# Kernel tuning notes

Hardware: AMD Instinct MI355X
Metric: run time of the kernel (lower is better)

The kernel has to match this reference:

```python
import jax, jax.numpy as jnp
import numpy as np

V, LAG, H, M, O, B = 32, 1024, 512, 1024, 1, 256


def setup_inputs() -> dict:
    key = jax.random.key(0)
    ks = jax.random.split(key, 10)
    s_ih = 1.0 / np.sqrt(H)
    inputs = jax.random.normal(ks[0], (B, V, LAG, 1), dtype=jnp.float32)
    # per-variable LSTMCell params, stacked over vars; gate order i,f,g,o (torch)
    W_ih = jax.random.uniform(ks[1], (V, 4 * H, LAG), minval=-s_ih, maxval=s_ih, dtype=jnp.float32)
    W_hh = jax.random.uniform(ks[2], (V, 4 * H, H), minval=-s_ih, maxval=s_ih, dtype=jnp.float32)
    b_ih = jax.random.uniform(ks[3], (V, 4 * H), minval=-s_ih, maxval=s_ih, dtype=jnp.float32)
    b_hh = jax.random.uniform(ks[4], (V, 4 * H), minval=-s_ih, maxval=s_ih, dtype=jnp.float32)
    imp_weights = jnp.asarray(np.ones((V,), np.float32) / V + np.random.RandomState(0).normal(0, 1e-5, (V,)).astype(np.float32))
    # xavier-normal linears, bias 0.1 (init_weights)
    mlp1_w = jax.random.normal(ks[5], (M, V * H), dtype=jnp.float32) * np.sqrt(2.0 / (V * H + M))
    mlp1_b = jnp.full((M,), 0.1, dtype=jnp.float32)
    mlp2_w = jax.random.normal(ks[6], (O, M), dtype=jnp.float32) * np.sqrt(2.0 / (M + O))
    mlp2_b = jnp.full((O,), 0.1, dtype=jnp.float32)
    return dict(inputs=inputs, W_ih=W_ih, W_hh=W_hh, b_ih=b_ih, b_hh=b_hh,
                imp_weights=imp_weights, mlp1_w=mlp1_w, mlp1_b=mlp1_b,
                mlp2_w=mlp2_w, mlp2_b=mlp2_b)


def reference(inputs, W_ih, W_hh, b_ih, b_hh, imp_weights, mlp1_w, mlp1_b, mlp2_w, mlp2_b):
    b = inputs.shape[0]
    x = inputs.reshape(b, V, LAG)                      # [B,V,LAG] (view in torch)
    h0 = jnp.zeros((b, V, H), inputs.dtype)           # initial states are zeros
    # single LSTMCell step for all vars at once; gate order i,f,g,o
    gates = (jnp.einsum('bvl,vgl->bvg', x, W_ih)
             + jnp.einsum('bvh,vgh->bvg', h0, W_hh)
             + b_ih[None] + b_hh[None])                # [B,V,4H]
    i, f, g, o = jnp.split(gates, 4, axis=-1)
    c = jax.nn.sigmoid(f) * 0.0 + jax.nn.sigmoid(i) * jnp.tanh(g)  # c0 = 0
    # original aggregates the CELL state (lstm_state[1]) weighted per variable
    agg = (c * imp_weights[None, :, None]).reshape(b, V * H)
    hid = jax.nn.relu(agg @ mlp1_w.T + mlp1_b)
    return hid @ mlp2_w.T + mlp2_b
```

## Files before the change

### kernel.cpp

```cpp
#include <hip/hip_runtime.h>
#include <hip/hip_bf16.h>
#include <stdint.h>

#define NVAR 32
#define LAGD 1024
#define BATCH 256
#define HDIM 512
#define SPLIT 32

typedef __attribute__((ext_vector_type(4))) float f32x4;
typedef __attribute__((ext_vector_type(8))) short short8;
typedef __attribute__((ext_vector_type(4))) unsigned short us4;
typedef __attribute__((ext_vector_type(8))) unsigned short us8;

__device__ __forceinline__ unsigned short f2bf(float f) {
  union { __hip_bfloat16 b; unsigned short s; } cv;
  cv.b = __float2bfloat16(f);
  return cv.s;
}
__device__ __forceinline__ us8 cvt8(f32x4 a, f32x4 b) {
  us8 u;
#pragma unroll
  for (int e = 0; e < 4; ++e) { u[e] = f2bf(a[e]); u[4 + e] = f2bf(b[e]); }
  return u;
}

__device__ __forceinline__ void gload16(const void* g, const void* l) {
  __builtin_amdgcn_global_load_lds(
      (const __attribute__((address_space(1))) unsigned int*)(uintptr_t)g,
      (__attribute__((address_space(3))) unsigned int*)(unsigned int)(uintptr_t)l,
      16, 0, 0);
}

__device__ __forceinline__ f32x4 gldx4(const float* p) {
  f32x4 r;
  asm volatile("global_load_dwordx4 %0, %1, off" : "=v"(r) : "v"(p) : "memory");
  return r;
}

#define WAITVM(N) do { \
    asm volatile("s_waitcnt vmcnt(" #N ")" ::: "memory"); \
    __builtin_amdgcn_sched_barrier(0); } while (0)

__device__ __forceinline__ void sync_ds() {
  asm volatile("s_waitcnt lgkmcnt(0)" ::: "memory");
  __builtin_amdgcn_s_barrier();
}

__global__ __launch_bounds__(256) void k0_tileX(
    const float* __restrict__ X,
    unsigned short* __restrict__ Xbf)
{
  const int v = blockIdx.x >> 5, kt = (blockIdx.x >> 1) & 15, mh = blockIdx.x & 1;
  const int t = threadIdx.x;
  const int rt = (mh << 7) + (t >> 3), c8 = (t & 7) << 3;
  const float* src = X + (size_t)rt * (NVAR * LAGD) + (size_t)v * LAGD + kt * 64 + c8;
  char* dst = (char*)Xbf + ((size_t)v * 16 + kt) * 32768;
#pragma unroll
  for (int p = 0; p < 4; ++p) {
    const int r = (p << 5) + rt;
    f32x4 a = *(const f32x4*)(src + (size_t)(p << 5) * (NVAR * LAGD));
    f32x4 b = *(const f32x4*)(src + (size_t)(p << 5) * (NVAR * LAGD) + 4);
    *(us8*)(dst + (((r << 7) + (c8 << 1)) ^ ((r & 7) << 4))) = cvt8(a, b);
  }
}

__global__ __launch_bounds__(512, 4) void k1_gates(
    const unsigned short* __restrict__ Xbf,
    const float* __restrict__ W,
    const float* __restrict__ b_ih,
    const float* __restrict__ b_hh,
    const float* __restrict__ imp,
    unsigned short* __restrict__ aggT)
{
  const int bid = blockIdx.x;
  const int chunk = ((bid & 7) << 6) | (bid >> 3);
  const int v = chunk >> 4;
  const int h0 = (chunk & 15) << 5;

  const int t = threadIdx.x, lane = t & 63, wave = t >> 6;
  const int wm = wave & 3, wh = wave >> 2;

  __shared__ __align__(16) unsigned char smem[81920];

  const char* Asrc = (const char*)Xbf + (size_t)v * 16 * 32768 + wave * 1024 + lane * 16;
  const unsigned aoff = wave * 1024u;

  const int brow = t >> 3;
  const int wrow = (brow < 32) ? (h0 + brow) : (1024 + h0 + brow - 32);
  const float* Bsrc = W + (size_t)v * (2048 * LAGD) + (size_t)wrow * LAGD + ((t & 7) << 3);
  const unsigned bwoff = (unsigned)(((brow << 7) + ((t & 7) << 4)) ^ ((brow & 7) << 4));

  f32x4 acc_i[4] = {}, acc_g[4] = {};
  f32x4 pbA[2], pbB[2];

#define GLA(BUF, KT) do { \
    _Pragma("unroll") for (int _r = 0; _r < 4; ++_r) \
      gload16(Asrc + (KT) * 32768 + _r * 8192, \
              smem + (BUF) * 32768u + aoff + _r * 8192); } while (0)

#define BLOAD(PB, KT) do { \
    (PB)[0] = gldx4(Bsrc + (KT) * 64); \
    (PB)[1] = gldx4(Bsrc + (KT) * 64 + 4); } while (0)

#define BSTORE(BUF, PB) \
    *(us8*)(smem + 65536u + (BUF) * 8192u + bwoff) = cvt8((PB)[0], (PB)[1])

#define COMP(BUF) do { \
    const unsigned char* Ab = smem + (BUF) * 32768u; \
    const unsigned char* Bb = smem + 65536u + (BUF) * 8192u; \
    const int fr = lane & 15, k16 = (lane >> 4) << 4; \
    _Pragma("unroll") for (int kk = 0; kk < 2; ++kk) { \
      short8 a[4], fi, fg; \
      _Pragma("unroll") for (int i = 0; i < 4; ++i) { \
        const int rw = (wm << 6) + (i << 4) + fr; \
        a[i] = *(const short8*)(Ab + (((rw << 7) + (kk << 6) + k16) ^ ((rw & 7) << 4))); \
      } \
      { const int rw = (wh << 4) + fr; \
        fi = *(const short8*)(Bb + (((rw << 7) + (kk << 6) + k16) ^ ((rw & 7) << 4))); \
        fg = *(const short8*)(Bb + ((((rw + 32) << 7) + (kk << 6) + k16) ^ ((rw & 7) << 4))); } \
      _Pragma("unroll") for (int i = 0; i < 4; ++i) { \
        acc_i[i] = __builtin_amdgcn_mfma_f32_16x16x32_bf16(a[i], fi, acc_i[i], 0, 0, 0); \
        acc_g[i] = __builtin_amdgcn_mfma_f32_16x16x32_bf16(a[i], fg, acc_g[i], 0, 0, 0); } \
    } } while (0)

#define STEP(CUR, NXT, PBP, PBN, KT) do { \
    GLA(NXT, (KT) + 1); \
    BLOAD(PBN, (KT) + 2); \
    COMP(CUR); \
    WAITVM(6);   \
    BSTORE(NXT, PBP); \
    WAITVM(2);   \
    sync_ds(); } while (0)

  GLA(0, 0);
  BLOAD(pbA, 0);
  BLOAD(pbB, 1);
  WAITVM(2);
  BSTORE(0, pbA);
  sync_ds();

#pragma unroll
  for (int kt = 0; kt < 14; kt += 2) {
    STEP(0, 1, pbB, pbA, kt);
    STEP(1, 0, pbA, pbB, kt + 1);
  }
  GLA(1, 15);
  COMP(0);
  WAITVM(4);
  BSTORE(1, pbB);
  WAITVM(0);
  sync_ds();
  COMP(1);

  const int col16 = lane & 15, row4 = (lane >> 4) << 2;
  const float impv = imp[v];
  const int h = h0 + (wh << 4) + col16;
  const float bsi = b_ih[v * 2048 + h] + b_hh[v * 2048 + h];
  const float bsg = b_ih[v * 2048 + 1024 + h] + b_hh[v * 2048 + 1024 + h];
  char* obase = (char*)aggT + ((size_t)v * 8 + (h >> 6)) * 32768;
  const int hc = h & 63;
#pragma unroll
  for (int i = 0; i < 4; ++i)
#pragma unroll
    for (int r = 0; r < 4; ++r) {
      const int m = (wm << 6) + (i << 4) + row4 + r;
      const float ii = acc_i[i][r] + bsi;
      const float gg = acc_g[i][r] + bsg;
      const float c = (1.0f / (1.0f + __expf(-ii))) * tanhf(gg) * impv;
      *(unsigned short*)(obase + (((m << 7) + (hc << 1)) ^ ((m & 7) << 4))) = f2bf(c);
    }
#undef STEP
#undef COMP
#undef GLA
#undef BLOAD
#undef BSTORE
}

__global__ __launch_bounds__(512, 4) void k3_mlp1(
    const unsigned short* __restrict__ aggT,
    const float* __restrict__ Wm,
    unsigned short* __restrict__ part)
{
  const int bid = blockIdx.x;
  const int chunk = ((bid & 7) << 6) | (bid >> 3);
  const int s = chunk >> 4;
  const int n0 = (chunk & 15) << 6;

  const int t = threadIdx.x, lane = t & 63, wave = t >> 6;
  const int wm = wave & 3, wn = wave >> 2;

  __shared__ __align__(16) unsigned char smem[81920];

  const char* Asrc = (const char*)aggT + (size_t)s * 8 * 32768 + wave * 1024 + lane * 16;
  const unsigned aoff = wave * 1024u;

  const int brow = t >> 3;
  const float* Bsrc = Wm + (size_t)(n0 + brow) * 16384 + (size_t)s * 512 + ((t & 7) << 3);
  const unsigned bwoff = (unsigned)(((brow << 7) + ((t & 7) << 4)) ^ ((brow & 7) << 4));

  f32x4 acc[4][2] = {};
  f32x4 pbA[2], pbB[2];

#define GLA(BUF, KT) do { \
    _Pragma("unroll") for (int _r = 0; _r < 4; ++_r) \
      gload16(Asrc + (KT) * 32768 + _r * 8192, \
              smem + (BUF) * 32768u + aoff + _r * 8192); } while (0)

#define BLOAD(PB, KT) do { \
    (PB)[0] = gldx4(Bsrc + (KT) * 64); \
    (PB)[1] = gldx4(Bsrc + (KT) * 64 + 4); } while (0)

#define BSTORE(BUF, PB) \
    *(us8*)(smem + 65536u + (BUF) * 8192u + bwoff) = cvt8((PB)[0], (PB)[1])

#define COMP(BUF) do { \
    const unsigned char* Ab = smem + (BUF) * 32768u; \
    const unsigned char* Bb = smem + 65536u + (BUF) * 8192u; \
    const int fr = lane & 15, k16 = (lane >> 4) << 4; \
    _Pragma("unroll") for (int kk = 0; kk < 2; ++kk) { \
      short8 a[4], b[2]; \
      _Pragma("unroll") for (int i = 0; i < 4; ++i) { \
        const int rw = (wm << 6) + (i << 4) + fr; \
        a[i] = *(const short8*)(Ab + (((rw << 7) + (kk << 6) + k16) ^ ((rw & 7) << 4))); \
      } \
      _Pragma("unroll") for (int j = 0; j < 2; ++j) { \
        const int rw = (wn << 5) + (j << 4) + fr; \
        b[j] = *(const short8*)(Bb + (((rw << 7) + (kk << 6) + k16) ^ ((rw & 7) << 4))); \
      } \
      _Pragma("unroll") for (int i = 0; i < 4; ++i) \
        _Pragma("unroll") for (int j = 0; j < 2; ++j) \
          acc[i][j] = __builtin_amdgcn_mfma_f32_16x16x32_bf16(a[i], b[j], acc[i][j], 0, 0, 0); \
    } } while (0)

#define STEP(CUR, NXT, PBP, PBN, KT) do { \
    GLA(NXT, (KT) + 1); \
    BLOAD(PBN, (KT) + 2); \
    COMP(CUR); \
    WAITVM(6); \
    BSTORE(NXT, PBP); \
    WAITVM(2); \
    sync_ds(); } while (0)

  GLA(0, 0);
  BLOAD(pbA, 0);
  BLOAD(pbB, 1);
  WAITVM(2);
  BSTORE(0, pbA);
  sync_ds();

#pragma unroll
  for (int kt = 0; kt < 6; kt += 2) {
    STEP(0, 1, pbB, pbA, kt);
    STEP(1, 0, pbA, pbB, kt + 1);
  }
  GLA(1, 7);
  COMP(0);
  WAITVM(4);
  BSTORE(1, pbB);
  WAITVM(0);
  sync_ds();
  COMP(1);

  const int col16 = lane & 15, row4 = (lane >> 4) << 2;
  unsigned short* outp = part + (size_t)s * BATCH * 1024;
#pragma unroll
  for (int i = 0; i < 4; ++i)
#pragma unroll
    for (int j = 0; j < 2; ++j)
#pragma unroll
      for (int r = 0; r < 4; ++r)
        outp[(size_t)((wm << 6) + (i << 4) + row4 + r) * 1024
             + n0 + (wn << 5) + (j << 4) + col16] = f2bf(acc[i][j][r]);
#undef STEP
#undef COMP
#undef GLA
#undef BLOAD
#undef BSTORE
}

__global__ __launch_bounds__(512) void k4_head(
    const unsigned short* __restrict__ part,
    const float* __restrict__ b1,
    const float* __restrict__ w2,
    const float* __restrict__ b2,
    float* __restrict__ out)
{
  const int b = blockIdx.x;
  const int t = threadIdx.x;
  const int n0 = t << 1;
  float s0 = b1[n0], s1 = b1[n0 + 1];
#pragma unroll 8
  for (int sp = 0; sp < SPLIT; ++sp) {
    const unsigned u = *(const unsigned*)(part + ((size_t)sp * BATCH + b) * 1024 + n0);
    union { unsigned u; float f; } lo, hi;
    lo.u = u << 16;
    hi.u = u & 0xffff0000u;
    s0 += lo.f;
    s1 += hi.f;
  }
  float accum = fmaxf(s0, 0.0f) * w2[n0] + fmaxf(s1, 0.0f) * w2[n0 + 1];
  __shared__ float red[8];
#pragma unroll
  for (int off = 32; off > 0; off >>= 1)
    accum += __shfl_down(accum, off);
  if ((t & 63) == 0) red[t >> 6] = accum;
  __syncthreads();
  if (t == 0) {
    float r = b2[0];
#pragma unroll
    for (int w = 0; w < 8; ++w) r += red[w];
    out[b] = r;
  }
}

extern "C" void kernel_launch(void* const* d_in, const int* in_sizes, int n_in,
                              void* d_out, int out_size, void* d_ws, size_t ws_size,
                              hipStream_t stream) {
  const float* inputs = (const float*)d_in[0];
  const float* W_ih   = (const float*)d_in[1];
  const float* b_ih   = (const float*)d_in[3];
  const float* b_hh   = (const float*)d_in[4];
  const float* imp    = (const float*)d_in[5];
  const float* m1w    = (const float*)d_in[6];
  const float* m1b    = (const float*)d_in[7];
  const float* m2w    = (const float*)d_in[8];
  const float* m2b    = (const float*)d_in[9];
  float* out = (float*)d_out;

  char* ws = (char*)d_ws;
  unsigned short* Xbf  = (unsigned short*)ws;
  unsigned short* aggT = (unsigned short*)(ws + (16u << 20));
  unsigned short* part = (unsigned short*)(ws + (24u << 20));

  k0_tileX<<<dim3(1024), 256, 0, stream>>>(inputs, Xbf);
  k1_gates<<<dim3(512), 512, 0, stream>>>(Xbf, W_ih, b_ih, b_hh, imp, aggT);
  k3_mlp1 <<<dim3(512), 512, 0, stream>>>(aggT, m1w, part);
  k4_head <<<dim3(256), 512, 0, stream>>>(part, m1b, m2w, m2b, out);
}
```

Before: 73.95 us.

## Fuse X bf16 conversion into gates kernel and halve MLP1 split-K

Removes the separate X tiling/conversion kernel. The gates kernel now loads fp32 inputs directly into registers, converts them to bf16 and stores them swizzled into LDS, which drops one launch and the round trip of the bf16 copy through global memory. The price is that each gates block re-reads and converts X itself, once per h-chunk, instead of reading a precomputed bf16 tile. Separately, MLP1 changes its split from 32×64 to 16×32, giving a longer K loop and narrower N tiles. That halves the partial sums the head kernel has to reduce, at the cost of fewer MFMAs per A-tile load.

After: 69.21 us, median of 2. 1.07x faster.

```diff
diff --git a/kernel.cpp b/kernel.cpp
--- a/kernel.cpp
+++ b/kernel.cpp
@@ -6,7 +6,7 @@
 #define LAGD 1024
 #define BATCH 256
 #define HDIM 512
-#define SPLIT 32
+#define SPLIT 16
 
 typedef __attribute__((ext_vector_type(4))) float f32x4;
 typedef __attribute__((ext_vector_type(8))) short short8;
@@ -22,6 +22,12 @@
   us8 u;
 #pragma unroll
   for (int e = 0; e < 4; ++e) { u[e] = f2bf(a[e]); u[4 + e] = f2bf(b[e]); }
+  return u;
+}
+__device__ __forceinline__ us4 cvt4(f32x4 a) {
+  us4 u;
+#pragma unroll
+  for (int e = 0; e < 4; ++e) u[e] = f2bf(a[e]);
   return u;
 }
 
@@ -47,26 +53,8 @@
   __builtin_amdgcn_s_barrier();
 }
 
-__global__ __launch_bounds__(256) void k0_tileX(
+__global__ __launch_bounds__(512, 4) void k1_gates(
     const float* __restrict__ X,
-    unsigned short* __restrict__ Xbf)
-{
-  const int v = blockIdx.x >> 5, kt = (blockIdx.x >> 1) & 15, mh = blockIdx.x & 1;
-  const int t = threadIdx.x;
-  const int rt = (mh << 7) + (t >> 3), c8 = (t & 7) << 3;
-  const float* src = X + (size_t)rt * (NVAR * LAGD) + (size_t)v * LAGD + kt * 64 + c8;
-  char* dst = (char*)Xbf + ((size_t)v * 16 + kt) * 32768;
-#pragma unroll
-  for (int p = 0; p < 4; ++p) {
-    const int r = (p << 5) + rt;
-    f32x4 a = *(const f32x4*)(src + (size_t)(p << 5) * (NVAR * LAGD));
-    f32x4 b = *(const f32x4*)(src + (size_t)(p << 5) * (NVAR * LAGD) + 4);
-    *(us8*)(dst + (((r << 7) + (c8 << 1)) ^ ((r & 7) << 4))) = cvt8(a, b);
-  }
-}
-
-__global__ __launch_bounds__(512, 4) void k1_gates(
-    const unsigned short* __restrict__ Xbf,
     const float* __restrict__ W,
     const float* __restrict__ b_ih,
     const float* __restrict__ b_hh,
@@ -83,8 +71,9 @@
 
   __shared__ __align__(16) unsigned char smem[81920];
 
-  const char* Asrc = (const char*)Xbf + (size_t)v * 16 * 32768 + wave * 1024 + lane * 16;
-  const unsigned aoff = wave * 1024u;
+  const int rt = t >> 3, c8 = (t & 7) << 3;
+  const float* Asrc = X + (size_t)rt * (NVAR * LAGD) + (size_t)v * LAGD + c8;
+  const unsigned awoff = (unsigned)(((rt << 7) + (c8 << 1)) ^ ((rt & 7) << 4));
 
   const int brow = t >> 3;
   const int wrow = (brow < 32) ? (h0 + brow) : (1024 + h0 + brow - 32);
@@ -92,12 +81,18 @@
   const unsigned bwoff = (unsigned)(((brow << 7) + ((t & 7) << 4)) ^ ((brow & 7) << 4));
 
   f32x4 acc_i[4] = {}, acc_g[4] = {};
-  f32x4 pbA[2], pbB[2];
-
-#define GLA(BUF, KT) do { \
-    _Pragma("unroll") for (int _r = 0; _r < 4; ++_r) \
-      gload16(Asrc + (KT) * 32768 + _r * 8192, \
-              smem + (BUF) * 32768u + aoff + _r * 8192); } while (0)
+  f32x4 pa[4][2], pbA[2], pbB[2];
+
+#define ALOAD(KT) do { \
+    _Pragma("unroll") for (int _p = 0; _p < 4; ++_p) { \
+      pa[_p][0] = gldx4(Asrc + (size_t)_p * 64 * (NVAR * LAGD) + (KT) * 64); \
+      pa[_p][1] = gldx4(Asrc + (size_t)_p * 64 * (NVAR * LAGD) + (KT) * 64 + 4); \
+    } } while (0)
+
+#define ASTORE(BUF) do { \
+    _Pragma("unroll") for (int _p = 0; _p < 4; ++_p) \
+      *(us8*)(smem + (BUF) * 32768u + awoff + _p * 8192u) = cvt8(pa[_p][0], pa[_p][1]); \
+  } while (0)
 
 #define BLOAD(PB, KT) do { \
     (PB)[0] = gldx4(Bsrc + (KT) * 64); \
@@ -125,18 +120,19 @@
     } } while (0)
 
 #define STEP(CUR, NXT, PBP, PBN, KT) do { \
-    GLA(NXT, (KT) + 1); \
-    BLOAD(PBN, (KT) + 2); \
+    ALOAD((KT) + 1);         \
+    BLOAD(PBN, (KT) + 2);    \
     COMP(CUR); \
-    WAITVM(6);   \
+    WAITVM(2);    \
+    ASTORE(NXT); \
     BSTORE(NXT, PBP); \
-    WAITVM(2);   \
     sync_ds(); } while (0)
 
-  GLA(0, 0);
+  ALOAD(0);
   BLOAD(pbA, 0);
   BLOAD(pbB, 1);
   WAITVM(2);
+  ASTORE(0);
   BSTORE(0, pbA);
   sync_ds();
 
@@ -145,11 +141,11 @@
     STEP(0, 1, pbB, pbA, kt);
     STEP(1, 0, pbA, pbB, kt + 1);
   }
-  GLA(1, 15);
+  ALOAD(15);
   COMP(0);
-  WAITVM(4);
+  WAITVM(0);
+  ASTORE(1);
   BSTORE(1, pbB);
-  WAITVM(0);
   sync_ds();
   COMP(1);
 
@@ -172,7 +168,8 @@
     }
 #undef STEP
 #undef COMP
-#undef GLA
+#undef ALOAD
+#undef ASTORE
 #undef BLOAD
 #undef BSTORE
 }
@@ -184,81 +181,75 @@
 {
   const int bid = blockIdx.x;
   const int chunk = ((bid & 7) << 6) | (bid >> 3);
-  const int s = chunk >> 4;
-  const int n0 = (chunk & 15) << 6;
+  const int s = chunk >> 5;
+  const int n0 = (chunk & 31) << 5;
 
   const int t = threadIdx.x, lane = t & 63, wave = t >> 6;
   const int wm = wave & 3, wn = wave >> 2;
 
-  __shared__ __align__(16) unsigned char smem[81920];
-
-  const char* Asrc = (const char*)aggT + (size_t)s * 8 * 32768 + wave * 1024 + lane * 16;
+  __shared__ __align__(16) unsigned char smem[73728];
+
+  const char* Asrc = (const char*)aggT + (size_t)s * 16 * 32768 + wave * 1024 + lane * 16;
   const unsigned aoff = wave * 1024u;
 
-  const int brow = t >> 3;
-  const float* Bsrc = Wm + (size_t)(n0 + brow) * 16384 + (size_t)s * 512 + ((t & 7) << 3);
-  const unsigned bwoff = (unsigned)(((brow << 7) + ((t & 7) << 4)) ^ ((brow & 7) << 4));
-
-  f32x4 acc[4][2] = {};
-  f32x4 pbA[2], pbB[2];
+  const int brow = t >> 4;
+  const int bcol = (t & 15) << 2;
+  const float* Bsrc = Wm + (size_t)(n0 + brow) * 16384 + (size_t)s * 1024 + bcol;
+  const unsigned bwoff = (unsigned)(((brow << 7) + (bcol << 1)) ^ ((brow & 7) << 4));
+
+  f32x4 acc[4] = {};
+  f32x4 pbA, pbB;
 
 #define GLA(BUF, KT) do { \
     _Pragma("unroll") for (int _r = 0; _r < 4; ++_r) \
       gload16(Asrc + (KT) * 32768 + _r * 8192, \
               smem + (BUF) * 32768u + aoff + _r * 8192); } while (0)
 
-#define BLOAD(PB, KT) do { \
-    (PB)[0] = gldx4(Bsrc + (KT) * 64); \
-    (PB)[1] = gldx4(Bsrc + (KT) * 64 + 4); } while (0)
+#define BLOAD(PB, KT) (PB) = gldx4(Bsrc + (KT) * 64)
 
 #define BSTORE(BUF, PB) \
-    *(us8*)(smem + 65536u + (BUF) * 8192u + bwoff) = cvt8((PB)[0], (PB)[1])
+    *(us4*)(smem + 65536u + (BUF) * 4096u + bwoff) = cvt4(PB)
 
 #define COMP(BUF) do { \
     const unsigned char* Ab = smem + (BUF) * 32768u; \
-    const unsigned char* Bb = smem + 65536u + (BUF) * 8192u; \
+    const unsigned char* Bb = smem + 65536u + (BUF) * 4096u; \
     const int fr = lane & 15, k16 = (lane >> 4) << 4; \
     _Pragma("unroll") for (int kk = 0; kk < 2; ++kk) { \
-      short8 a[4], b[2]; \
+      short8 a[4], bfr; \
       _Pragma("unroll") for (int i = 0; i < 4; ++i) { \
         const int rw = (wm << 6) + (i << 4) + fr; \
         a[i] = *(const short8*)(Ab + (((rw << 7) + (kk << 6) + k16) ^ ((rw & 7) << 4))); \
       } \
-      _Pragma("unroll") for (int j = 0; j < 2; ++j) { \
-        const int rw = (wn << 5) + (j << 4) + fr; \
-        b[j] = *(const short8*)(Bb + (((rw << 7) + (kk << 6) + k16) ^ ((rw & 7) << 4))); \
-      } \
+      { const int rw = (wn << 4) + fr; \
+        bfr = *(const short8*)(Bb + (((rw << 7) + (kk << 6) + k16) ^ ((rw & 7) << 4))); } \
       _Pragma("unroll") for (int i = 0; i < 4; ++i) \
-        _Pragma("unroll") for (int j = 0; j < 2; ++j) \
-          acc[i][j] = __builtin_amdgcn_mfma_f32_16x16x32_bf16(a[i], b[j], acc[i][j], 0, 0, 0); \
+        acc[i] = __builtin_amdgcn_mfma_f32_16x16x32_bf16(a[i], bfr, acc[i], 0, 0, 0); \
     } } while (0)
 
 #define STEP(CUR, NXT, PBP, PBN, KT) do { \
-    GLA(NXT, (KT) + 1); \
-    BLOAD(PBN, (KT) + 2); \
+    GLA(NXT, (KT) + 1);      \
+    BLOAD(PBN, (KT) + 2);    \
     COMP(CUR); \
-    WAITVM(6); \
+    WAITVM(1);    \
     BSTORE(NXT, PBP); \
-    WAITVM(2); \
     sync_ds(); } while (0)
 
   GLA(0, 0);
   BLOAD(pbA, 0);
   BLOAD(pbB, 1);
-  WAITVM(2);
+  WAITVM(1);
   BSTORE(0, pbA);
   sync_ds();
 
 #pragma unroll
-  for (int kt = 0; kt < 6; kt += 2) {
+  for (int kt = 0; kt < 14; kt += 2) {
     STEP(0, 1, pbB, pbA, kt);
     STEP(1, 0, pbA, pbB, kt + 1);
   }
-  GLA(1, 7);
+  GLA(1, 15);
   COMP(0);
-  WAITVM(4);
+  WAITVM(0);
   BSTORE(1, pbB);
-  WAITVM(0);
   sync_ds();
   COMP(1);
 
@@ -267,11 +258,9 @@
 #pragma unroll
   for (int i = 0; i < 4; ++i)
 #pragma unroll
-    for (int j = 0; j < 2; ++j)
-#pragma unroll
-      for (int r = 0; r < 4; ++r)
-        outp[(size_t)((wm << 6) + (i << 4) + row4 + r) * 1024
-             + n0 + (wn << 5) + (j << 4) + col16] = f2bf(acc[i][j][r]);
+    for (int r = 0; r < 4; ++r)
+      outp[(size_t)((wm << 6) + (i << 4) + row4 + r) * 1024
+           + n0 + (wn << 4) + col16] = f2bf(acc[i][r]);
 #undef STEP
 #undef COMP
 #undef GLA
@@ -290,7 +279,7 @@
   const int t = threadIdx.x;
   const int n0 = t << 1;
   float s0 = b1[n0], s1 = b1[n0 + 1];
-#pragma unroll 8
+#pragma unroll
   for (int sp = 0; sp < SPLIT; ++sp) {
     const unsigned u = *(const unsigned*)(part + ((size_t)sp * BATCH + b) * 1024 + n0);
     union { unsigned u; float f; } lo, hi;
@@ -329,12 +318,10 @@
   float* out = (float*)d_out;
 
   char* ws = (char*)d_ws;
-  unsigned short* Xbf  = (unsigned short*)ws;
-  unsigned short* aggT = (unsigned short*)(ws + (16u << 20));
-  unsigned short* part = (unsigned short*)(ws + (24u << 20));
-
-  k0_tileX<<<dim3(1024), 256, 0, stream>>>(inputs, Xbf);
-  k1_gates<<<dim3(512), 512, 0, stream>>>(Xbf, W_ih, b_ih, b_hh, imp, aggT);
+  unsigned short* aggT = (unsigned short*)ws;
+  unsigned short* part = (unsigned short*)(ws + (8u << 20));
+
+  k1_gates<<<dim3(512), 512, 0, stream>>>(inputs, W_ih, b_ih, b_hh, imp, aggT);
   k3_mlp1 <<<dim3(512), 512, 0, stream>>>(aggT, m1w, part);
   k4_head <<<dim3(256), 512, 0, stream>>>(part, m1b, m2w, m2b, out);
 }
```
